# Performance work log

Hardware: AMD Instinct MI355X
Metric: run time of the kernel (lower is better)

Reference implementation:

```python
import jax, jax.numpy as jnp
import numpy as np

N = 50000
E = 800000
IN_C, HID_C, OUT_C = 512, 128, 256


def setup_inputs() -> dict:
    key = jax.random.key(0)
    k1, k2, k3, k4, k5, k6 = jax.random.split(key, 6)
    x = jax.random.normal(k1, (N, IN_C), dtype=jnp.float32)
    edge_index = jax.random.randint(k2, (2, E), 0, N, dtype=jnp.int64)
    # Linear weights stored torch-style as [out, in]; bias per layer
    w1 = jax.random.normal(k3, (HID_C, IN_C), dtype=jnp.float32) * (1.0 / np.sqrt(IN_C))
    b1 = jax.random.normal(k4, (HID_C,), dtype=jnp.float32) * 0.02
    w2 = jax.random.normal(k5, (OUT_C, HID_C), dtype=jnp.float32) * (1.0 / np.sqrt(HID_C))
    b2 = jax.random.normal(k6, (OUT_C,), dtype=jnp.float32) * 0.02
    return {"x": x, "edge_index": edge_index, "w1": w1, "b1": b1, "w2": w2, "b2": b2}


def gcn_conv(x, edge_index, w, b):
    # x: [N, Cin], w: [Cout, Cin] (torch Linear layout), b: [Cout]
    h = x @ w.T                              # [N, Cout]
    src, dst = edge_index[0], edge_index[1]
    msgs = h[src]                            # gather: [E, Cout]
    agg = jax.ops.segment_sum(msgs, dst, num_segments=h.shape[0])  # scatter_add
    return agg + b


def reference(x, edge_index, w1, b1, w2, b2):
    h = gcn_conv(x, edge_index, w1, b1)
    h = jax.nn.relu(h)
    out = gcn_conv(h, edge_index, w2, b2)
    return out
```

## Files before the change

kernel.cpp:

```cpp
#include <hip/hip_runtime.h>

#define NN 50000
#define EE 800000
#define INC 512
#define HIDC 128
#define OUTC 256
#define CAP 64
#define OV_CAP 65536
#define BUILD_BLOCKS 196
#define GB1 782

typedef __attribute__((ext_vector_type(8))) short bf16x8;
typedef __attribute__((ext_vector_type(4))) float f32x4;

__device__ __forceinline__ short f2bf(float f) {
    unsigned u = __float_as_uint(f);
    unsigned r = u + 0x7fff + ((u >> 16) & 1);
    return (short)(r >> 16);
}
__device__ __forceinline__ float bf2f(short s) {
    return __uint_as_float(((unsigned)(unsigned short)s) << 16);
}

template<bool IN_BF16, bool ADDBIAS, bool OUT_BF16>
__device__ __forceinline__ void gemm_core(
    const void* __restrict__ Av, const float* __restrict__ B,
    const float* __restrict__ bias, void* __restrict__ Cv,
    int M, int Nc, int K, int bx, int by,
    short As[64][72], short Bs[128][72])
{
    int tid = threadIdx.x;
    int lane = tid & 63, wave = tid >> 6;
    int row0 = bx * 64, col0 = by * 128;
    int wm = (wave & 1) * 32, wn = (wave >> 1) * 64;
    int l16 = lane & 15, quad = lane >> 4;

    f32x4 acc[2][4];
#pragma unroll
    for (int i = 0; i < 2; i++)
#pragma unroll
        for (int j = 0; j < 4; j++) acc[i][j] = {0.f, 0.f, 0.f, 0.f};

    for (int k0 = 0; k0 < K; k0 += 64) {
        if (IN_BF16) {
            const short* A = (const short*)Av;
#pragma unroll
            for (int w = 0; w < 2; w++) {
                int f = tid + w * 256;
                int rr = f >> 3, c8 = f & 7;
                int gr = row0 + rr;
                bf16x8 v = {0, 0, 0, 0, 0, 0, 0, 0};
                if (gr < M) v = *(const bf16x8*)&A[(long)gr * K + k0 + c8 * 8];
                *(bf16x8*)&As[rr][c8 * 8] = v;
            }
        } else {
            const float* A = (const float*)Av;
#pragma unroll
            for (int w = 0; w < 4; w++) {
                int f = tid + w * 256;
                int rr = f >> 4, c4 = f & 15;
                int gr = row0 + rr;
                float4 v = make_float4(0.f, 0.f, 0.f, 0.f);
                if (gr < M) v = *(const float4*)&A[(long)gr * K + k0 + c4 * 4];
                short4 s;
                s.x = f2bf(v.x); s.y = f2bf(v.y); s.z = f2bf(v.z); s.w = f2bf(v.w);
                *(short4*)&As[rr][c4 * 4] = s;
            }
        }
#pragma unroll
        for (int w = 0; w < 8; w++) {
            int f = tid + w * 256;
            int rr = f >> 4, c4 = f & 15;
            float4 v = *(const float4*)&B[(long)(col0 + rr) * K + k0 + c4 * 4];
            short4 s;
            s.x = f2bf(v.x); s.y = f2bf(v.y); s.z = f2bf(v.z); s.w = f2bf(v.w);
            *(short4*)&Bs[rr][c4 * 4] = s;
        }
        __syncthreads();

#pragma unroll
        for (int kk = 0; kk < 64; kk += 32) {
            bf16x8 af[2], bfr[4];
#pragma unroll
            for (int i = 0; i < 2; i++)
                af[i] = *(const bf16x8*)&As[wm + i * 16 + l16][kk + quad * 8];
#pragma unroll
            for (int j = 0; j < 4; j++)
                bfr[j] = *(const bf16x8*)&Bs[wn + j * 16 + l16][kk + quad * 8];
#pragma unroll
            for (int i = 0; i < 2; i++)
#pragma unroll
                for (int j = 0; j < 4; j++)
                    acc[i][j] = __builtin_amdgcn_mfma_f32_16x16x32_bf16(
                        af[i], bfr[j], acc[i][j], 0, 0, 0);
        }
        __syncthreads();
    }

#pragma unroll
    for (int i = 0; i < 2; i++) {
#pragma unroll
        for (int rr = 0; rr < 4; rr++) {
            int grow = row0 + wm + i * 16 + quad * 4 + rr;
            if (grow < M) {
#pragma unroll
                for (int j = 0; j < 4; j++) {
                    int gcol = col0 + wn + j * 16 + l16;
                    float v = acc[i][j][rr];
                    if (ADDBIAS) v += bias[gcol];
                    if (OUT_BF16)
                        ((short*)Cv)[(long)grow * Nc + gcol] = f2bf(v);
                    else
                        ((float*)Cv)[(long)grow * Nc + gcol] = v;
                }
            }
        }
    }
}

__global__ __launch_bounds__(256) void fat_build_gemm1(
    const int* __restrict__ ei, int* __restrict__ cnt,
    unsigned short* __restrict__ bucket, int* __restrict__ ovcnt,
    int* __restrict__ ovlist,
    const float* __restrict__ x, const float* __restrict__ w1,
    short* __restrict__ h)
{
    __shared__ short As[64][72];
    __shared__ short Bs[128][72];

    if (blockIdx.x < BUILD_BLOCKS) {
        int t = threadIdx.x;
        long base = ((long)blockIdx.x * 256 + t) * 16;
        if (base + 16 <= EE) {
            int4 sv[4], dv[4];
#pragma unroll
            for (int q = 0; q < 4; q++) {
                sv[q] = *(const int4*)&ei[base + q * 4];
                dv[q] = *(const int4*)&ei[EE + base + q * 4];
            }
            const int* sp = (const int*)sv;
            const int* dp = (const int*)dv;
#pragma unroll
            for (int k = 0; k < 16; k++) {
                int src = sp[k], dst = dp[k];
                int pos = atomicAdd(&cnt[dst], 1);
                if (pos < CAP) bucket[(long)dst * CAP + pos] = (unsigned short)src;
                else {
                    int o = atomicAdd(ovcnt, 1);
                    if (o < OV_CAP) { ovlist[o * 2] = src; ovlist[o * 2 + 1] = dst; }
                }
            }
        } else {
            for (int k = 0; k < 16; k++) {
                long e = base + k;
                if (e < EE) {
                    int src = ei[e], dst = ei[EE + e];
                    int pos = atomicAdd(&cnt[dst], 1);
                    if (pos < CAP) bucket[(long)dst * CAP + pos] = (unsigned short)src;
                    else {
                        int o = atomicAdd(ovcnt, 1);
                        if (o < OV_CAP) { ovlist[o * 2] = src; ovlist[o * 2 + 1] = dst; }
                    }
                }
            }
        }
    } else {
        gemm_core<false, false, true>(x, w1, nullptr, h, NN, HIDC, INC,
                                      blockIdx.x - BUILD_BLOCKS, 0, As, Bs);
    }
}

__global__ __launch_bounds__(256) void gemm2_k(
    const short* __restrict__ r2, const float* __restrict__ w2,
    const float* __restrict__ b2, float* __restrict__ out)
{
    __shared__ short As[64][72];
    __shared__ short Bs[128][72];
    gemm_core<true, true, false>(r2, w2, b2, out, NN, OUTC, HIDC,
                                 blockIdx.x, blockIdx.y, As, Bs);
}

template<bool RELU>
__global__ __launch_bounds__(256) void gather_k(
    const short* __restrict__ hsrc, const unsigned short* __restrict__ bucket,
    const int* __restrict__ cnt, const int* __restrict__ ovcnt,
    const int* __restrict__ ovlist, const float* __restrict__ bias,
    short* __restrict__ rout)
{
    int wave = threadIdx.x >> 6;
    int lane = threadIdx.x & 63;
    int sub = lane >> 4, c8 = lane & 15;

#pragma unroll
    for (int it = 0; it < 4; it++) {
        int node = blockIdx.x * 16 + wave * 4 + it;
        int m0 = cnt[node];
        int m = m0 > CAP ? CAP : m0;
        const unsigned short* bk = bucket + (long)node * CAP;

        float acc[8];
#pragma unroll
        for (int k = 0; k < 8; k++) acc[k] = 0.f;

        int j = 0;
        for (; j + 16 <= m; j += 16) {
            int s0 = bk[j + sub];
            int s1 = bk[j + 4 + sub];
            int s2 = bk[j + 8 + sub];
            int s3 = bk[j + 12 + sub];
            bf16x8 v0 = *(const bf16x8*)&hsrc[((long)s0 << 7) + c8 * 8];
            bf16x8 v1 = *(const bf16x8*)&hsrc[((long)s1 << 7) + c8 * 8];
            bf16x8 v2 = *(const bf16x8*)&hsrc[((long)s2 << 7) + c8 * 8];
            bf16x8 v3 = *(const bf16x8*)&hsrc[((long)s3 << 7) + c8 * 8];
#pragma unroll
            for (int k = 0; k < 8; k++)
                acc[k] += bf2f(v0[k]) + bf2f(v1[k]) + bf2f(v2[k]) + bf2f(v3[k]);
        }
        for (; j < m; j += 4) {
            int e = j + sub;
            if (e < m) {
                int s0 = bk[e];
                bf16x8 v0 = *(const bf16x8*)&hsrc[((long)s0 << 7) + c8 * 8];
#pragma unroll
                for (int k = 0; k < 8; k++) acc[k] += bf2f(v0[k]);
            }
        }

        if (m0 > CAP && sub == 0) {
            int n = *ovcnt; if (n > OV_CAP) n = OV_CAP;
            for (int i = 0; i < n; i++) {
                if (ovlist[i * 2 + 1] == node) {
                    bf16x8 v0 =
                        *(const bf16x8*)&hsrc[((long)ovlist[i * 2] << 7) + c8 * 8];
#pragma unroll
                    for (int k = 0; k < 8; k++) acc[k] += bf2f(v0[k]);
                }
            }
        }

#pragma unroll
        for (int k = 0; k < 8; k++) {
            acc[k] += __shfl_xor(acc[k], 16);
            acc[k] += __shfl_xor(acc[k], 32);
        }

        if (sub == 0) {
            bf16x8 o;
            if (RELU) {
#pragma unroll
                for (int k = 0; k < 8; k++)
                    o[k] = f2bf(fmaxf(acc[k] + bias[c8 * 8 + k], 0.f));
            } else {
#pragma unroll
                for (int k = 0; k < 8; k++) o[k] = f2bf(acc[k]);
            }
            *(bf16x8*)&rout[((long)node << 7) + c8 * 8] = o;
        }
    }
}

extern "C" void kernel_launch(void* const* d_in, const int* in_sizes, int n_in,
                              void* d_out, int out_size, void* d_ws, size_t ws_size,
                              hipStream_t stream) {
    const float* x  = (const float*)d_in[0];
    const int*   ei = (const int*)d_in[1];
    const float* w1 = (const float*)d_in[2];
    const float* b1 = (const float*)d_in[3];
    const float* w2 = (const float*)d_in[4];
    const float* b2 = (const float*)d_in[5];
    float* out = (float*)d_out;

    char* ws = (char*)d_ws;
    size_t off = 0;
    short* h    = (short*)(ws + off); off += (size_t)NN * HIDC * 2;
    short* r    = (short*)(ws + off); off += (size_t)NN * HIDC * 2;
    short* r2   = (short*)(ws + off); off += (size_t)NN * HIDC * 2;
    unsigned short* bucket = (unsigned short*)(ws + off);
    off += (size_t)NN * CAP * 2;
    int* cnt    = (int*)(ws + off);   off += (size_t)NN * 4;
    int* ovcnt  = (int*)(ws + off);   off += 256;
    int* ovlist = (int*)(ws + off);   off += (size_t)OV_CAP * 2 * 4;

    hipMemsetAsync(cnt, 0, (size_t)NN * 4 + 4, stream);

    dim3 blk(256);

    fat_build_gemm1<<<dim3(BUILD_BLOCKS + GB1), blk, 0, stream>>>(
        ei, cnt, bucket, ovcnt, ovlist, x, w1, h);

    gather_k<true><<<dim3(3125), blk, 0, stream>>>(
        h, bucket, cnt, ovcnt, ovlist, b1, r);

    gather_k<false><<<dim3(3125), blk, 0, stream>>>(
        r, bucket, cnt, ovcnt, ovlist, nullptr, r2);

    gemm2_k<<<dim3(GB1, 2), blk, 0, stream>>>(r2, w2, b2, out);
}
```

Baseline: 307.0 us.

## Split gather into four column-slice passes with nontemporal index loads and stores

Each gather now covers a 32-column slice of the 128-wide hidden features and is launched four times per layer. Each wave spreads 16 edges across lanes, with 4 lanes per edge, so the slice working set is smaller and more likely to stay in cache. Index loads and output stores become nontemporal. In exchange, the bucket lists are read four times, launch count rises, and each lane loads only one edge per iteration instead of four, which lowers memory-level parallelism.

```diff
diff --git a/kernel.cpp b/kernel.cpp
--- a/kernel.cpp
+++ b/kernel.cpp
@@ -12,6 +12,7 @@
 
 typedef __attribute__((ext_vector_type(8))) short bf16x8;
 typedef __attribute__((ext_vector_type(4))) float f32x4;
+typedef __attribute__((ext_vector_type(4))) int i32x4;
 
 __device__ __forceinline__ short f2bf(float f) {
     unsigned u = __float_as_uint(f);
@@ -185,11 +186,11 @@
     const short* __restrict__ hsrc, const unsigned short* __restrict__ bucket,
     const int* __restrict__ cnt, const int* __restrict__ ovcnt,
     const int* __restrict__ ovlist, const float* __restrict__ bias,
-    short* __restrict__ rout)
+    short* __restrict__ rout, int c0)
 {
     int wave = threadIdx.x >> 6;
     int lane = threadIdx.x & 63;
-    int sub = lane >> 4, c8 = lane & 15;
+    int sub = lane >> 2, c4 = lane & 3;
 
 #pragma unroll
     for (int it = 0; it < 4; it++) {
@@ -204,23 +205,16 @@
 
         int j = 0;
         for (; j + 16 <= m; j += 16) {
-            int s0 = bk[j + sub];
-            int s1 = bk[j + 4 + sub];
-            int s2 = bk[j + 8 + sub];
-            int s3 = bk[j + 12 + sub];
-            bf16x8 v0 = *(const bf16x8*)&hsrc[((long)s0 << 7) + c8 * 8];
-            bf16x8 v1 = *(const bf16x8*)&hsrc[((long)s1 << 7) + c8 * 8];
-            bf16x8 v2 = *(const bf16x8*)&hsrc[((long)s2 << 7) + c8 * 8];
-            bf16x8 v3 = *(const bf16x8*)&hsrc[((long)s3 << 7) + c8 * 8];
-#pragma unroll
-            for (int k = 0; k < 8; k++)
-                acc[k] += bf2f(v0[k]) + bf2f(v1[k]) + bf2f(v2[k]) + bf2f(v3[k]);
-        }
-        for (; j < m; j += 4) {
+            int s0 = __builtin_nontemporal_load(&bk[j + sub]);
+            bf16x8 v0 = *(const bf16x8*)&hsrc[((long)s0 << 7) + c0 + c4 * 8];
+#pragma unroll
+            for (int k = 0; k < 8; k++) acc[k] += bf2f(v0[k]);
+        }
+        if (j < m) {
             int e = j + sub;
             if (e < m) {
-                int s0 = bk[e];
-                bf16x8 v0 = *(const bf16x8*)&hsrc[((long)s0 << 7) + c8 * 8];
+                int s0 = __builtin_nontemporal_load(&bk[e]);
+                bf16x8 v0 = *(const bf16x8*)&hsrc[((long)s0 << 7) + c0 + c4 * 8];
 #pragma unroll
                 for (int k = 0; k < 8; k++) acc[k] += bf2f(v0[k]);
             }
@@ -230,8 +224,8 @@
             int n = *ovcnt; if (n > OV_CAP) n = OV_CAP;
             for (int i = 0; i < n; i++) {
                 if (ovlist[i * 2 + 1] == node) {
-                    bf16x8 v0 =
-                        *(const bf16x8*)&hsrc[((long)ovlist[i * 2] << 7) + c8 * 8];
+                    bf16x8 v0 = *(const bf16x8*)
+                        &hsrc[((long)ovlist[i * 2] << 7) + c0 + c4 * 8];
 #pragma unroll
                     for (int k = 0; k < 8; k++) acc[k] += bf2f(v0[k]);
                 }
@@ -240,6 +234,8 @@
 
 #pragma unroll
         for (int k = 0; k < 8; k++) {
+            acc[k] += __shfl_xor(acc[k], 4);
+            acc[k] += __shfl_xor(acc[k], 8);
             acc[k] += __shfl_xor(acc[k], 16);
             acc[k] += __shfl_xor(acc[k], 32);
         }
@@ -249,12 +245,14 @@
             if (RELU) {
 #pragma unroll
                 for (int k = 0; k < 8; k++)
-                    o[k] = f2bf(fmaxf(acc[k] + bias[c8 * 8 + k], 0.f));
+                    o[k] = f2bf(fmaxf(acc[k] + bias[c0 + c4 * 8 + k], 0.f));
             } else {
 #pragma unroll
                 for (int k = 0; k < 8; k++) o[k] = f2bf(acc[k]);
             }
-            *(bf16x8*)&rout[((long)node << 7) + c8 * 8] = o;
+            union { bf16x8 v; i32x4 i; } pun; pun.v = o;
+            __builtin_nontemporal_store(
+                pun.i, (i32x4*)&rout[((long)node << 7) + c0 + c4 * 8]);
         }
     }
 }
@@ -288,11 +286,13 @@
     fat_build_gemm1<<<dim3(BUILD_BLOCKS + GB1), blk, 0, stream>>>(
         ei, cnt, bucket, ovcnt, ovlist, x, w1, h);
 
-    gather_k<true><<<dim3(3125), blk, 0, stream>>>(
-        h, bucket, cnt, ovcnt, ovlist, b1, r);
-
-    gather_k<false><<<dim3(3125), blk, 0, stream>>>(
-        r, bucket, cnt, ovcnt, ovlist, nullptr, r2);
+    for (int p = 0; p < 4; p++)
+        gather_k<true><<<dim3(3125), blk, 0, stream>>>(
+            h, bucket, cnt, ovcnt, ovlist, b1, r, p * 32);
+
+    for (int p = 0; p < 4; p++)
+        gather_k<false><<<dim3(3125), blk, 0, stream>>>(
+            r, bucket, cnt, ovcnt, ovlist, nullptr, r2, p * 32);
 
     gemm2_k<<<dim3(GB1, 2), blk, 0, stream>>>(r2, w2, b2, out);
 }
```

Result: slower. 436.8 us (+42.3%).
